# Optimization experiments

Hardware: AMD Instinct MI355X
Metric: run time of the kernel (lower is better)

The kernel has to match this reference:

```python
import jax, jax.numpy as jnp
import numpy as np

B, C, H, W = 2, 256, 64, 64
NUM_HEADS = 4
DIM_HEAD_QK = 64
DIM_HEAD_V = 64  # dim_out // num_heads
DIM_OUT_QK = NUM_HEADS * DIM_HEAD_QK  # 256
DIM_OUT_V = NUM_HEADS * DIM_HEAD_V    # 256
SCALE = DIM_HEAD_QK ** -0.5


def rel_logits_1d(q, rel_k, permute):
    # q: (Bh, Hq, Wq, d), rel_k: (2*Wq-1, d)
    Bh, Hq, Wq, d = q.shape
    R = 2 * Wq - 1
    x = jnp.einsum('bhwd,rd->bhwr', q, rel_k)              # (Bh, Hq, Wq, R)
    x = x.reshape(-1, Wq, R)
    x_pad = jnp.pad(x, ((0, 0), (0, 0), (0, 1))).reshape(x.shape[0], -1)
    x_pad = jnp.pad(x_pad, ((0, 0), (0, Wq - 1)))
    x_pad = x_pad.reshape(-1, Wq + 1, R)
    x = x_pad[:, :Wq, Wq - 1:]                              # (Bh*Hq, Wq, Wq)
    x = x.reshape(Bh, Hq, 1, Wq, Wq)
    x = jnp.broadcast_to(x, (Bh, Hq, Hq, Wq, Wq))
    return jnp.transpose(x, permute)


def pos_embed_rel(q, height_rel, width_rel):
    # q: (Bh, HW, d)
    Bh = q.shape[0]
    qr = q.reshape(Bh, H, W, -1)
    rel_w = rel_logits_1d(qr, width_rel, (0, 1, 3, 2, 4))   # (Bh, H, W, H, W)
    qt = jnp.transpose(qr, (0, 2, 1, 3))                    # (Bh, W, H, d)
    rel_h = rel_logits_1d(qt, height_rel, (0, 3, 1, 4, 2))  # (Bh, H, W, H, W)
    return (rel_h + rel_w).reshape(Bh, H * W, H * W)


def setup_inputs() -> dict:
    key = jax.random.key(0)
    k1, k2, k3, k4 = jax.random.split(key, 4)
    x = jax.random.normal(k1, (B, C, H, W), dtype=jnp.float32)
    qkv_w = jax.random.normal(k2, (2 * DIM_OUT_QK + DIM_OUT_V, C), dtype=jnp.float32) * (C ** -0.5)
    height_rel = jax.random.normal(k3, (2 * H - 1, DIM_HEAD_QK), dtype=jnp.float32) * SCALE
    width_rel = jax.random.normal(k4, (2 * W - 1, DIM_HEAD_QK), dtype=jnp.float32) * SCALE
    return {"x": x, "qkv_w": qkv_w, "height_rel": height_rel, "width_rel": width_rel}


def reference(x, qkv_w, height_rel, width_rel):
    # 1x1 conv == channel matmul
    qkv = jnp.einsum('bchw,oc->bohw', x, qkv_w)             # (B, 768, H, W)
    q, k, v = jnp.split(qkv, [DIM_OUT_QK, 2 * DIM_OUT_QK], axis=1)
    HW = H * W
    q = q.reshape(B * NUM_HEADS, DIM_HEAD_QK, HW).transpose(0, 2, 1)  # (Bh, HW, d)
    k = k.reshape(B * NUM_HEADS, DIM_HEAD_QK, HW)                     # (Bh, d, HW)
    v = v.reshape(B * NUM_HEADS, DIM_HEAD_V, HW).transpose(0, 2, 1)   # (Bh, HW, dv)
    attn = jnp.einsum('bnd,bdm->bnm', q, k) * SCALE + pos_embed_rel(q, height_rel, width_rel)
    attn = jax.nn.softmax(attn, axis=-1)
    out = jnp.einsum('bnm,bmd->bnd', attn, v)               # (Bh, HW, dv)
    out = out.transpose(0, 2, 1).reshape(B, DIM_OUT_V, H, W)
    return out
```

## Files before the change

### kernel.cpp

```cpp
#include <hip/hip_runtime.h>
#include <hip/hip_bf16.h>

typedef __attribute__((ext_vector_type(8))) short bf16x8;
typedef __attribute__((ext_vector_type(4))) float f32x4;

static __device__ __forceinline__ f32x4 mfma16(bf16x8 a, bf16x8 b, f32x4 c) {
    return __builtin_amdgcn_mfma_f32_16x16x32_bf16(a, b, c, 0, 0, 0);
}
static __device__ __forceinline__ void gll16(const void* g, void* l) {
    __builtin_amdgcn_global_load_lds(
        (const __attribute__((address_space(1))) unsigned int*)g,
        (__attribute__((address_space(3))) unsigned int*)l, 16, 0, 0);
}

#define LOG2E 1.44269504f

__global__ __launch_bounds__(256, 4) void qkv_kernel(
    const float* __restrict__ x, const float* __restrict__ w,
    __hip_bfloat16* __restrict__ qb, __hip_bfloat16* __restrict__ kb,
    __hip_bfloat16* __restrict__ vt)
{
    alignas(16) __shared__ __hip_bfloat16 sA[64 * 72];
    alignas(16) __shared__ __hip_bfloat16 sB[64 * 72];
    const int nb = blockIdx.x * 64;
    const int ob = blockIdx.y * 64;
    const int b  = blockIdx.z;
    const int tid  = threadIdx.x;
    const int lane = tid & 63;
    const int wv   = tid >> 6;
    const int quad = lane >> 4;
    const int l16  = lane & 15;

    f32x4 acc[4];
    for (int i = 0; i < 4; i++) acc[i] = (f32x4)0.f;

    const int oA = tid >> 2, cA = (tid & 3) << 4;
    const float* srcw = w + (ob + oA) * 256 + cA;
    const int cB = tid >> 2, nB = (tid & 3) << 4;
    const int csw = cB ^ ((tid & 3) * 16);
    const float* srcx = x + ((size_t)b * 256 + cB) * 4096 + nb + nB;

    float4 ra[4], rb4[4];
    #pragma unroll
    for (int i = 0; i < 4; i++) ra[i]  = *(const float4*)(srcw + i * 4);
    #pragma unroll
    for (int i = 0; i < 4; i++) rb4[i] = *(const float4*)(srcx + i * 4);

    for (int t = 0; t < 4; t++) {
        __syncthreads();
        {
            union { bf16x8 v; __hip_bfloat16 h[8]; } u0, u1;
            #pragma unroll
            for (int i = 0; i < 2; i++) {
                float4 f = ra[i];
                u0.h[4*i+0] = __float2bfloat16(f.x); u0.h[4*i+1] = __float2bfloat16(f.y);
                u0.h[4*i+2] = __float2bfloat16(f.z); u0.h[4*i+3] = __float2bfloat16(f.w);
            }
            #pragma unroll
            for (int i = 0; i < 2; i++) {
                float4 f = ra[2 + i];
                u1.h[4*i+0] = __float2bfloat16(f.x); u1.h[4*i+1] = __float2bfloat16(f.y);
                u1.h[4*i+2] = __float2bfloat16(f.z); u1.h[4*i+3] = __float2bfloat16(f.w);
            }
            *(bf16x8*)&sA[oA * 72 + cA]     = u0.v;
            *(bf16x8*)&sA[oA * 72 + cA + 8] = u1.v;
        }
        {
            #pragma unroll
            for (int i = 0; i < 4; i++) {
                float4 f = rb4[i];
                sB[(nB + 4*i + 0) * 72 + csw] = __float2bfloat16(f.x);
                sB[(nB + 4*i + 1) * 72 + csw] = __float2bfloat16(f.y);
                sB[(nB + 4*i + 2) * 72 + csw] = __float2bfloat16(f.z);
                sB[(nB + 4*i + 3) * 72 + csw] = __float2bfloat16(f.w);
            }
        }
        __syncthreads();
        if (t < 3) {
            #pragma unroll
            for (int i = 0; i < 4; i++)
                ra[i]  = *(const float4*)(srcw + (t + 1) * 64 + i * 4);
            #pragma unroll
            for (int i = 0; i < 4; i++)
                rb4[i] = *(const float4*)(srcx + (size_t)(t + 1) * 64 * 4096 + i * 4);
        }
        const __hip_bfloat16* aRow = &sA[(16 * wv + l16) * 72];
        #pragma unroll
        for (int ks = 0; ks < 2; ks++) {
            bf16x8 af = *(const bf16x8*)&aRow[ks * 32 + quad * 8];
            #pragma unroll
            for (int ct = 0; ct < 4; ct++) {
                bf16x8 bfv = *(const bf16x8*)&sB[(16 * ct + l16) * 72
                                                 + ((ks * 32 + quad * 8) ^ (ct * 16))];
                acc[ct] = mfma16(af, bfv, acc[ct]);
            }
        }
    }
    if (ob < 512) {
        __syncthreads();
        #pragma unroll
        for (int ct = 0; ct < 4; ct++) {
            union { short4 s; __hip_bfloat16 hh[4]; } u;
            #pragma unroll
            for (int r = 0; r < 4; r++) u.hh[r] = __float2bfloat16(acc[ct][r]);
            *(short4*)&sA[(16 * ct + l16) * 72 + 16 * wv + 4 * quad] = u.s;
        }
        __syncthreads();
        const int n_l = tid >> 2, d16 = (tid & 3) * 16;
        const int n = nb + n_l;
        const __hip_bfloat16* srcl = &sA[n_l * 72 + d16];
        bf16x8 v0 = *(const bf16x8*)srcl;
        bf16x8 v1 = *(const bf16x8*)(srcl + 8);
        const int bhh = b * 4 + ((ob & 255) >> 6);
        if (ob < 256) {
            __hip_bfloat16* dst = qb + ((size_t)bhh * 4096 + n) * 64;
            *(bf16x8*)(dst + d16)     = v0;
            *(bf16x8*)(dst + d16 + 8) = v1;
        } else {
            const int s = (n & 7) << 3;
            __hip_bfloat16* dst = kb + ((size_t)bhh * 4096 + n) * 64;
            *(bf16x8*)(dst + (d16 ^ s))       = v0;
            *(bf16x8*)(dst + ((d16 + 8) ^ s)) = v1;
        }
    } else {
        __syncthreads();
        #pragma unroll
        for (int ct = 0; ct < 4; ct++)
            #pragma unroll
            for (int r = 0; r < 4; r++)
                sA[(16 * wv + quad * 4 + r) * 72 + 16 * ct + l16] = __float2bfloat16(acc[ct][r]);
        int o2 = (ob - 512) + 16 * wv + l16;
        int bhh = b * 4 + (o2 >> 6), d = o2 & 63;
        const __hip_bfloat16* srcl = &sA[(16 * wv + l16) * 72 + 16 * quad];
        __hip_bfloat16* vrow = vt + ((size_t)bhh * 64 + d) * 4096;
        const int kt = quad & 1;
        const int gbase = nb + (quad >> 1) * 32;
        const int dsw = (d & 7) << 3;
        #pragma unroll
        for (int m = 0; m < 4; m++) {
            short4 val = *(const short4*)(srcl + 4 * m);
            int P4 = gbase + 8 * m + 4 * kt;
            *(short4*)(vrow + (P4 ^ dsw)) = val;
        }
    }
}

__global__ __launch_bounds__(512, 4) void attn_kernel(
    const __hip_bfloat16* __restrict__ qb, const __hip_bfloat16* __restrict__ kb,
    const __hip_bfloat16* __restrict__ vt, const float* __restrict__ hrel,
    const float* __restrict__ wrel, float* __restrict__ out)
{
    extern __shared__ __align__(16) char smem[];
    alignas(16) __shared__ __hip_bfloat16 sRH[64 * 66];

    const int h    = blockIdx.x;
    const int bh   = blockIdx.y;
    const int tid  = threadIdx.x;
    const int lane = tid & 63;
    const int wv   = tid >> 6;
    const int qg   = wv >> 2;
    const int kg   = wv & 3;
    const int quad = lane >> 4;
    const int l16  = lane & 15;

    __hip_bfloat16* sQ   = (__hip_bfloat16*)smem;
    __hip_bfloat16* sW   = (__hip_bfloat16*)smem + 64 * 72;
    __hip_bfloat16* sHRs = (__hip_bfloat16*)smem + 192 * 72;
    __hip_bfloat16* sRWt = (__hip_bfloat16*)smem;

    {
        int r = tid >> 3, d8 = (tid & 7) * 8;
        *(bf16x8*)&sQ[r * 72 + d8] =
            *(const bf16x8*)&qb[(((size_t)bh * 4096 + h * 64 + r)) * 64 + d8];
    }
    {
        int r = tid >> 2, c0 = (tid & 3) << 4;
        union { bf16x8 v; __hip_bfloat16 h8[8]; } u0, u1;
        #pragma unroll
        for (int i = 0; i < 2; i++) {
            float4 f = (r < 127) ? *(const float4*)&wrel[r * 64 + c0 + 4*i] : float4{0,0,0,0};
            u0.h8[4*i+0] = __float2bfloat16(f.x); u0.h8[4*i+1] = __float2bfloat16(f.y);
            u0.h8[4*i+2] = __float2bfloat16(f.z); u0.h8[4*i+3] = __float2bfloat16(f.w);
        }
        #pragma unroll
        for (int i = 0; i < 2; i++) {
            float4 f = (r < 127) ? *(const float4*)&wrel[r * 64 + c0 + 8 + 4*i] : float4{0,0,0,0};
            u1.h8[4*i+0] = __float2bfloat16(f.x); u1.h8[4*i+1] = __float2bfloat16(f.y);
            u1.h8[4*i+2] = __float2bfloat16(f.z); u1.h8[4*i+3] = __float2bfloat16(f.w);
        }
        *(bf16x8*)&sW[r * 72 + c0]     = u0.v;
        *(bf16x8*)&sW[r * 72 + c0 + 8] = u1.v;
    }
    {
        int r = tid >> 3, c0 = (tid & 7) * 8;
        union { bf16x8 v; __hip_bfloat16 h8[8]; } u0;
        #pragma unroll
        for (int i = 0; i < 2; i++) {
            float4 f = *(const float4*)&hrel[(63 - h + r) * 64 + c0 + 4*i];
            u0.h8[4*i+0] = __float2bfloat16(f.x); u0.h8[4*i+1] = __float2bfloat16(f.y);
            u0.h8[4*i+2] = __float2bfloat16(f.z); u0.h8[4*i+3] = __float2bfloat16(f.w);
        }
        *(bf16x8*)&sHRs[r * 72 + c0] = u0.v;
    }
    __syncthreads();

    const int g    = wv & 3;
    const int half = wv >> 2;
    const __hip_bfloat16* aRow = &sQ[(16 * g + l16) * 72];
    bf16x8 qf0 = *(const bf16x8*)&aRow[quad * 8];
    bf16x8 qf1 = *(const bf16x8*)&aRow[32 + quad * 8];
    bf16x8 qm[2][2];
    #pragma unroll
    for (int qt = 0; qt < 2; qt++) {
        const __hip_bfloat16* qr = &sQ[(qg * 32 + 16 * qt + l16) * 72];
        qm[qt][0] = *(const bf16x8*)&qr[quad * 8];
        qm[qt][1] = *(const bf16x8*)&qr[32 + quad * 8];
    }
    __syncthreads();

    {
        const int rbase = half * 64;
        #pragma unroll
        for (int ct = 0; ct < 4; ct++) {
            int rr = rbase + 16 * ct + l16;
            f32x4 a = (f32x4)0.f;
            a = mfma16(qf0, *(const bf16x8*)&sW[rr * 72 + quad * 8], a);
            a = mfma16(qf1, *(const bf16x8*)&sW[rr * 72 + 32 + quad * 8], a);
            #pragma unroll
            for (int r = 0; r < 4; r++) {
                int ww = 16 * g + quad * 4 + r;
                int wp = rr + ww - 63;
                if (wp >= 0 && wp < 64) sRWt[ww * 68 + wp] = __float2bfloat16(a[r]);
            }
        }
    }
    if (half == 0) {
        #pragma unroll
        for (int ct = 0; ct < 4; ct++) {
            f32x4 a = (f32x4)0.f;
            a = mfma16(qf0, *(const bf16x8*)&sHRs[(16 * ct + l16) * 72 + quad * 8], a);
            a = mfma16(qf1, *(const bf16x8*)&sHRs[(16 * ct + l16) * 72 + 32 + quad * 8], a);
            #pragma unroll
            for (int r = 0; r < 4; r++)
                sRH[(16 * g + quad * 4 + r) * 66 + 16 * ct + l16] = __float2bfloat16(a[r]);
        }
    }
    __syncthreads();

    union S4 { short4 s; __hip_bfloat16 h[4]; };
    float rwf[2][2][4];
    #pragma unroll
    for (int qt = 0; qt < 2; qt++)
        #pragma unroll
        for (int kt = 0; kt < 2; kt++) {
            S4 t;
            t.s = *(const short4*)&sRWt[(qg * 32 + 16 * qt + l16) * 68
                                        + 32 * (kg & 1) + 16 * kt + 4 * quad];
            #pragma unroll
            for (int r = 0; r < 4; r++)
                rwf[qt][kt][r] = LOG2E * __bfloat162float(t.h[r]);
        }
    __syncthreads();

    const char* kT = (const char*)kb + (size_t)bh * 524288 + wv * 1024 + lane * 16;
    const char* vT = (const char*)vt + (size_t)bh * 524288
                     + (size_t)(wv * 4 + quad) * 8192 + l16 * 16;

    gll16(kT,           smem + wv * 1024);
    gll16(kT + 8192,    smem + 8192 + wv * 1024);
    gll16(vT,           smem + 16384 + wv * 1024);
    gll16(vT + 262144,  smem + 24576 + wv * 1024);
    __syncthreads();

    f32x4 oacc[2][4];
    #pragma unroll
    for (int qt = 0; qt < 2; qt++)
        #pragma unroll
        for (int dt = 0; dt < 4; dt++) oacc[qt][dt] = (f32x4)0.f;
    f32x4 lacc[2] = {(f32x4)0.f, (f32x4)0.f};
    const bf16x8 vones = (bf16x8)(short)0x3F80;

    const int krowOff = (kg * 32 + l16) * 128;
    const int sw  = (l16 & 7) << 4;
    const int kA  = (quad * 16) ^ sw;
    const int kB  = (64 + quad * 16) ^ sw;
    const int vOff = 16384 + l16 * 256 + ((kg * 64 + quad * 16) ^ sw);

    const __hip_bfloat16* rh0 = &sRH[(qg * 32 + l16) * 66];
    const __hip_bfloat16* rh1 = &sRH[(qg * 32 + 16 + l16) * 66];
    const float SC = 0.125f * LOG2E;

    for (int j = 0; j < 32; j++) {
        const char* buf = smem + (j & 1) * 32768;
        if (j < 31) {
            char* nbuf = smem + ((j + 1) & 1) * 32768;
            const char* gk = kT + (size_t)(j + 1) * 16384;
            gll16(gk,          nbuf + wv * 1024);
            gll16(gk + 8192,   nbuf + 8192 + wv * 1024);
            const char* gv = vT + (size_t)(j + 1) * 256;
            gll16(gv,          nbuf + 16384 + wv * 1024);
            gll16(gv + 262144, nbuf + 24576 + wv * 1024);
        }

        const char* kr = buf + krowOff;
        bf16x8 kf00 = *(const bf16x8*)(kr + kA);
        bf16x8 kf01 = *(const bf16x8*)(kr + kB);
        bf16x8 kf10 = *(const bf16x8*)(kr + 2048 + kA);
        bf16x8 kf11 = *(const bf16x8*)(kr + 2048 + kB);

        f32x4 s[2][2];
        __builtin_amdgcn_s_setprio(1);
        #pragma unroll
        for (int qt = 0; qt < 2; qt++) {
            f32x4 a0 = (f32x4)0.f, a1 = (f32x4)0.f;
            a0 = mfma16(kf00, qm[qt][0], a0);
            a0 = mfma16(kf01, qm[qt][1], a0);
            a1 = mfma16(kf10, qm[qt][0], a1);
            a1 = mfma16(kf11, qm[qt][1], a1);
            s[qt][0] = a0; s[qt][1] = a1;
        }
        __builtin_amdgcn_s_setprio(0);

        const int hp = 2 * j + (kg >> 1);
        bf16x8 pa[2];
        #pragma unroll
        for (int qt = 0; qt < 2; qt++) {
            float rhb = LOG2E * __bfloat162float((qt ? rh1 : rh0)[hp]);
            float pv[8];
            #pragma unroll
            for (int r = 0; r < 4; r++)
                pv[r] = __builtin_amdgcn_exp2f(fmaf(s[qt][0][r], SC, rwf[qt][0][r] + rhb));
            #pragma unroll
            for (int r = 0; r < 4; r++)
                pv[4 + r] = __builtin_amdgcn_exp2f(fmaf(s[qt][1][r], SC, rwf[qt][1][r] + rhb));
            union { bf16x8 v; __hip_bfloat162 b2[4]; } pu;
            #pragma unroll
            for (int pi = 0; pi < 4; pi++)
                pu.b2[pi] = __float22bfloat162_rn(float2{pv[2 * pi], pv[2 * pi + 1]});
            pa[qt] = pu.v;
        }

        __builtin_amdgcn_s_setprio(1);
        #pragma unroll
        for (int dt = 0; dt < 4; dt++) {
            bf16x8 vf = *(const bf16x8*)(buf + vOff + dt * 4096);
            oacc[0][dt] = mfma16(pa[0], vf, oacc[0][dt]);
            oacc[1][dt] = mfma16(pa[1], vf, oacc[1][dt]);
        }
        lacc[0] = mfma16(pa[0], vones, lacc[0]);
        lacc[1] = mfma16(pa[1], vones, lacc[1]);
        __builtin_amdgcn_s_setprio(0);
        __syncthreads();
    }

    float* obuf = (float*)smem;
    if (kg != 0) {
        float* rb = obuf + (kg - 1) * 4672;
        #pragma unroll
        for (int qt = 0; qt < 2; qt++)
            #pragma unroll
            for (int dt = 0; dt < 4; dt++)
                *(f32x4*)&rb[qg * 2304 + (16 * dt + l16) * 36 + 16 * qt + 4 * quad]
                    = oacc[qt][dt];
        if (l16 == 0)
            #pragma unroll
            for (int qt = 0; qt < 2; qt++)
                #pragma unroll
                for (int r = 0; r < 4; r++)
                    rb[4608 + qg * 32 + 16 * qt + 4 * quad + r] = lacc[qt][r];
    }
    __syncthreads();
    if (kg == 0) {
        #pragma unroll
        for (int rg = 0; rg < 3; rg++) {
            const float* rb = obuf + rg * 4672;
            #pragma unroll
            for (int qt = 0; qt < 2; qt++) {
                #pragma unroll
                for (int dt = 0; dt < 4; dt++)
                    oacc[qt][dt] += *(const f32x4*)&rb[qg * 2304 + (16 * dt + l16) * 36
                                                       + 16 * qt + 4 * quad];
                #pragma unroll
                for (int r = 0; r < 4; r++)
                    lacc[qt][r] += rb[4608 + qg * 32 + 16 * qt + 4 * quad + r];
            }
        }
        const int b = bh >> 2, head = bh & 3;
        #pragma unroll
        for (int qt = 0; qt < 2; qt++) {
            f32x4 lv;
            #pragma unroll
            for (int r = 0; r < 4; r++) lv[r] = 1.f / lacc[qt][r];
            #pragma unroll
            for (int dt = 0; dt < 4; dt++) {
                f32x4 o = oacc[qt][dt] * lv;
                int dv = 16 * dt + l16;
                int q0 = qg * 32 + 16 * qt + 4 * quad;
                *(f32x4*)&out[((size_t)(b * 256 + head * 64 + dv)) * 4096 + h * 64 + q0] = o;
            }
        }
    }
}

extern "C" void kernel_launch(void* const* d_in, const int* in_sizes, int n_in,
                              void* d_out, int out_size, void* d_ws, size_t ws_size,
                              hipStream_t stream) {
    const float* x     = (const float*)d_in[0];
    const float* qkv_w = (const float*)d_in[1];
    const float* hrel  = (const float*)d_in[2];
    const float* wrel  = (const float*)d_in[3];
    float* out = (float*)d_out;

    __hip_bfloat16* qb = (__hip_bfloat16*)d_ws;
    __hip_bfloat16* kb = qb + (size_t)8 * 4096 * 64;
    __hip_bfloat16* vt = kb + (size_t)8 * 4096 * 64;

    qkv_kernel<<<dim3(64, 12, 2), 256, 0, stream>>>(x, qkv_w, qb, kb, vt);
    attn_kernel<<<dim3(64, 8), 512, 65536, stream>>>(qb, kb, vt, hrel, wrel, out);
}
```

Before: 126.8 us.

## Halve attention block to 256 threads with two key groups and smaller LDS

The attention kernel moves from 8 waves (2 query groups x 4 key groups) to 4 waves (2 x 2), and halves the double-buffered K/V tile to 64 keys per iteration over 64 iterations. Dynamic LDS drops from 64KB to 32KB and the final cross-wave reduction covers only one partner group. The aim is to fit more blocks per CU and cut reduction overhead. The cost is half as many waves per block to hide latency, twice as many loop iterations and barriers, and relative-position tables built in two passes.

Measured after the change: 130.2 us. +2.7%, slower.

```diff
diff --git a/kernel.cpp b/kernel.cpp
--- a/kernel.cpp
+++ b/kernel.cpp
@@ -11,6 +11,14 @@
     __builtin_amdgcn_global_load_lds(
         (const __attribute__((address_space(1))) unsigned int*)g,
         (__attribute__((address_space(3))) unsigned int*)l, 16, 0, 0);
+}
+static __device__ __forceinline__ bf16x8 pack8(float4 a, float4 b) {
+    union { bf16x8 v; __hip_bfloat162 h[4]; } u;
+    u.h[0] = __float22bfloat162_rn(float2{a.x, a.y});
+    u.h[1] = __float22bfloat162_rn(float2{a.z, a.w});
+    u.h[2] = __float22bfloat162_rn(float2{b.x, b.y});
+    u.h[3] = __float22bfloat162_rn(float2{b.z, b.w});
+    return u.v;
 }
 
 #define LOG2E 1.44269504f
@@ -145,68 +153,43 @@
     }
 }
 
-__global__ __launch_bounds__(512, 4) void attn_kernel(
+__global__ __launch_bounds__(256, 4) void attn_kernel(
     const __hip_bfloat16* __restrict__ qb, const __hip_bfloat16* __restrict__ kb,
     const __hip_bfloat16* __restrict__ vt, const float* __restrict__ hrel,
     const float* __restrict__ wrel, float* __restrict__ out)
 {
     extern __shared__ __align__(16) char smem[];
-    alignas(16) __shared__ __hip_bfloat16 sRH[64 * 66];
+    __shared__ __hip_bfloat16 sRH[64 * 64];
 
     const int h    = blockIdx.x;
     const int bh   = blockIdx.y;
     const int tid  = threadIdx.x;
     const int lane = tid & 63;
     const int wv   = tid >> 6;
-    const int qg   = wv >> 2;
-    const int kg   = wv & 3;
+    const int qg   = wv >> 1;
+    const int kg   = wv & 1;
     const int quad = lane >> 4;
     const int l16  = lane & 15;
 
     __hip_bfloat16* sQ   = (__hip_bfloat16*)smem;
     __hip_bfloat16* sW   = (__hip_bfloat16*)smem + 64 * 72;
-    __hip_bfloat16* sHRs = (__hip_bfloat16*)smem + 192 * 72;
+    __hip_bfloat16* sHRs = (__hip_bfloat16*)smem + 128 * 72;
     __hip_bfloat16* sRWt = (__hip_bfloat16*)smem;
 
     {
-        int r = tid >> 3, d8 = (tid & 7) * 8;
-        *(bf16x8*)&sQ[r * 72 + d8] =
-            *(const bf16x8*)&qb[(((size_t)bh * 4096 + h * 64 + r)) * 64 + d8];
-    }
-    {
-        int r = tid >> 2, c0 = (tid & 3) << 4;
-        union { bf16x8 v; __hip_bfloat16 h8[8]; } u0, u1;
-        #pragma unroll
-        for (int i = 0; i < 2; i++) {
-            float4 f = (r < 127) ? *(const float4*)&wrel[r * 64 + c0 + 4*i] : float4{0,0,0,0};
-            u0.h8[4*i+0] = __float2bfloat16(f.x); u0.h8[4*i+1] = __float2bfloat16(f.y);
-            u0.h8[4*i+2] = __float2bfloat16(f.z); u0.h8[4*i+3] = __float2bfloat16(f.w);
-        }
-        #pragma unroll
-        for (int i = 0; i < 2; i++) {
-            float4 f = (r < 127) ? *(const float4*)&wrel[r * 64 + c0 + 8 + 4*i] : float4{0,0,0,0};
-            u1.h8[4*i+0] = __float2bfloat16(f.x); u1.h8[4*i+1] = __float2bfloat16(f.y);
-            u1.h8[4*i+2] = __float2bfloat16(f.z); u1.h8[4*i+3] = __float2bfloat16(f.w);
-        }
-        *(bf16x8*)&sW[r * 72 + c0]     = u0.v;
-        *(bf16x8*)&sW[r * 72 + c0 + 8] = u1.v;
-    }
-    {
-        int r = tid >> 3, c0 = (tid & 7) * 8;
-        union { bf16x8 v; __hip_bfloat16 h8[8]; } u0;
-        #pragma unroll
-        for (int i = 0; i < 2; i++) {
-            float4 f = *(const float4*)&hrel[(63 - h + r) * 64 + c0 + 4*i];
-            u0.h8[4*i+0] = __float2bfloat16(f.x); u0.h8[4*i+1] = __float2bfloat16(f.y);
-            u0.h8[4*i+2] = __float2bfloat16(f.z); u0.h8[4*i+3] = __float2bfloat16(f.w);
-        }
-        *(bf16x8*)&sHRs[r * 72 + c0] = u0.v;
+        int r = tid >> 2, c0 = (tid & 3) * 16;
+        const __hip_bfloat16* srcq = qb + ((size_t)bh * 4096 + h * 64 + r) * 64 + c0;
+        *(bf16x8*)&sQ[r * 72 + c0]     = *(const bf16x8*)srcq;
+        *(bf16x8*)&sQ[r * 72 + c0 + 8] = *(const bf16x8*)(srcq + 8);
+        const float* srch = hrel + (size_t)(63 - h + r) * 64 + c0;
+        *(bf16x8*)&sHRs[r * 72 + c0]     = pack8(*(const float4*)srch,
+                                                 *(const float4*)(srch + 4));
+        *(bf16x8*)&sHRs[r * 72 + c0 + 8] = pack8(*(const float4*)(srch + 8),
+                                                 *(const float4*)(srch + 12));
     }
     __syncthreads();
 
-    const int g    = wv & 3;
-    const int half = wv >> 2;
-    const __hip_bfloat16* aRow = &sQ[(16 * g + l16) * 72];
+    const __hip_bfloat16* aRow = &sQ[(16 * wv + l16) * 72];
     bf16x8 qf0 = *(const bf16x8*)&aRow[quad * 8];
     bf16x8 qf1 = *(const bf16x8*)&aRow[32 + quad * 8];
     bf16x8 qm[2][2];
@@ -218,34 +201,46 @@
     }
     __syncthreads();
 
-    {
-        const int rbase = half * 64;
+    for (int p = 0; p < 2; p++) {
+        {
+            int r = tid >> 2, c0 = (tid & 3) * 16;
+            int gr = 64 * p + r;
+            bf16x8 w0 = (bf16x8)(short)0, w1 = (bf16x8)(short)0;
+            if (gr < 127) {
+                const float* s = wrel + (size_t)gr * 64 + c0;
+                w0 = pack8(*(const float4*)s, *(const float4*)(s + 4));
+                w1 = pack8(*(const float4*)(s + 8), *(const float4*)(s + 12));
+            }
+            *(bf16x8*)&sW[r * 72 + c0]     = w0;
+            *(bf16x8*)&sW[r * 72 + c0 + 8] = w1;
+        }
+        __syncthreads();
         #pragma unroll
         for (int ct = 0; ct < 4; ct++) {
-            int rr = rbase + 16 * ct + l16;
             f32x4 a = (f32x4)0.f;
-            a = mfma16(qf0, *(const bf16x8*)&sW[rr * 72 + quad * 8], a);
-            a = mfma16(qf1, *(const bf16x8*)&sW[rr * 72 + 32 + quad * 8], a);
+            a = mfma16(qf0, *(const bf16x8*)&sW[(16 * ct + l16) * 72 + quad * 8], a);
+            a = mfma16(qf1, *(const bf16x8*)&sW[(16 * ct + l16) * 72 + 32 + quad * 8], a);
+            int rr = 64 * p + 16 * ct + l16;
             #pragma unroll
             for (int r = 0; r < 4; r++) {
-                int ww = 16 * g + quad * 4 + r;
+                int ww = 16 * wv + quad * 4 + r;
                 int wp = rr + ww - 63;
                 if (wp >= 0 && wp < 64) sRWt[ww * 68 + wp] = __float2bfloat16(a[r]);
             }
         }
-    }
-    if (half == 0) {
-        #pragma unroll
-        for (int ct = 0; ct < 4; ct++) {
-            f32x4 a = (f32x4)0.f;
-            a = mfma16(qf0, *(const bf16x8*)&sHRs[(16 * ct + l16) * 72 + quad * 8], a);
-            a = mfma16(qf1, *(const bf16x8*)&sHRs[(16 * ct + l16) * 72 + 32 + quad * 8], a);
-            #pragma unroll
-            for (int r = 0; r < 4; r++)
-                sRH[(16 * g + quad * 4 + r) * 66 + 16 * ct + l16] = __float2bfloat16(a[r]);
-        }
-    }
-    __syncthreads();
+        if (p == 0) {
+            #pragma unroll
+            for (int ct = 0; ct < 4; ct++) {
+                f32x4 a = (f32x4)0.f;
+                a = mfma16(qf0, *(const bf16x8*)&sHRs[(16 * ct + l16) * 72 + quad * 8], a);
+                a = mfma16(qf1, *(const bf16x8*)&sHRs[(16 * ct + l16) * 72 + 32 + quad * 8], a);
+                #pragma unroll
+                for (int r = 0; r < 4; r++)
+                    sRH[(16 * ct + l16) * 64 + 16 * wv + quad * 4 + r] = __float2bfloat16(a[r]);
+            }
+        }
+        __syncthreads();
+    }
 
     union S4 { short4 s; __hip_bfloat16 h[4]; };
     float rwf[2][2][4];
@@ -255,21 +250,21 @@
         for (int kt = 0; kt < 2; kt++) {
             S4 t;
             t.s = *(const short4*)&sRWt[(qg * 32 + 16 * qt + l16) * 68
-                                        + 32 * (kg & 1) + 16 * kt + 4 * quad];
+                                        + kg * 32 + 16 * kt + 4 * quad];
             #pragma unroll
             for (int r = 0; r < 4; r++)
                 rwf[qt][kt][r] = LOG2E * __bfloat162float(t.h[r]);
         }
     __syncthreads();
 
-    const char* kT = (const char*)kb + (size_t)bh * 524288 + wv * 1024 + lane * 16;
+    const char* kT = (const char*)kb + (size_t)bh * 524288 + wv * 2048 + lane * 16;
     const char* vT = (const char*)vt + (size_t)bh * 524288
-                     + (size_t)(wv * 4 + quad) * 8192 + l16 * 16;
-
-    gll16(kT,           smem + wv * 1024);
-    gll16(kT + 8192,    smem + 8192 + wv * 1024);
-    gll16(vT,           smem + 16384 + wv * 1024);
-    gll16(vT + 262144,  smem + 24576 + wv * 1024);
+                     + (size_t)(16 * wv + (lane >> 3)) * 8192 + (lane & 7) * 16;
+
+    gll16(kT,          smem + wv * 2048);
+    gll16(kT + 1024,   smem + wv * 2048 + 1024);
+    gll16(vT,          smem + 8192 + wv * 2048);
+    gll16(vT + 65536,  smem + 8192 + wv * 2048 + 1024);
     __syncthreads();
 
     f32x4 oacc[2][4];
@@ -284,22 +279,21 @@
     const int sw  = (l16 & 7) << 4;
     const int kA  = (quad * 16) ^ sw;
     const int kB  = (64 + quad * 16) ^ sw;
-    const int vOff = 16384 + l16 * 256 + ((kg * 64 + quad * 16) ^ sw);
-
-    const __hip_bfloat16* rh0 = &sRH[(qg * 32 + l16) * 66];
-    const __hip_bfloat16* rh1 = &sRH[(qg * 32 + 16 + l16) * 66];
+    const int vOff = 8192 + l16 * 128 + ((kg * 64 + quad * 16) ^ sw);
+
+    const __hip_bfloat16* rhq = sRH + qg * 32 + l16;
     const float SC = 0.125f * LOG2E;
 
-    for (int j = 0; j < 32; j++) {
-        const char* buf = smem + (j & 1) * 32768;
-        if (j < 31) {
-            char* nbuf = smem + ((j + 1) & 1) * 32768;
-            const char* gk = kT + (size_t)(j + 1) * 16384;
-            gll16(gk,          nbuf + wv * 1024);
-            gll16(gk + 8192,   nbuf + 8192 + wv * 1024);
-            const char* gv = vT + (size_t)(j + 1) * 256;
-            gll16(gv,          nbuf + 16384 + wv * 1024);
-            gll16(gv + 262144, nbuf + 24576 + wv * 1024);
+    for (int j = 0; j < 64; j++) {
+        const char* buf = smem + (j & 1) * 16384;
+        if (j < 63) {
+            char* nbuf = smem + ((j + 1) & 1) * 16384;
+            const char* gk = kT + (size_t)(j + 1) * 8192;
+            gll16(gk,         nbuf + wv * 2048);
+            gll16(gk + 1024,  nbuf + wv * 2048 + 1024);
+            const char* gv = vT + (size_t)(j + 1) * 128;
+            gll16(gv,         nbuf + 8192 + wv * 2048);
+            gll16(gv + 65536, nbuf + 8192 + wv * 2048 + 1024);
         }
 
         const char* kr = buf + krowOff;
@@ -321,11 +315,10 @@
         }
         __builtin_amdgcn_s_setprio(0);
 
-        const int hp = 2 * j + (kg >> 1);
         bf16x8 pa[2];
         #pragma unroll
         for (int qt = 0; qt < 2; qt++) {
-            float rhb = LOG2E * __bfloat162float((qt ? rh1 : rh0)[hp]);
+            float rhb = LOG2E * __bfloat162float(rhq[j * 64 + 16 * qt]);
             float pv[8];
             #pragma unroll
             for (int r = 0; r < 4; r++)
@@ -343,7 +336,7 @@
         __builtin_amdgcn_s_setprio(1);
         #pragma unroll
         for (int dt = 0; dt < 4; dt++) {
-            bf16x8 vf = *(const bf16x8*)(buf + vOff + dt * 4096);
+            bf16x8 vf = *(const bf16x8*)(buf + vOff + dt * 2048);
             oacc[0][dt] = mfma16(pa[0], vf, oacc[0][dt]);
             oacc[1][dt] = mfma16(pa[1], vf, oacc[1][dt]);
         }
@@ -354,36 +347,31 @@
     }
 
     float* obuf = (float*)smem;
-    if (kg != 0) {
-        float* rb = obuf + (kg - 1) * 4672;
+    if (kg == 1) {
         #pragma unroll
         for (int qt = 0; qt < 2; qt++)
             #pragma unroll
             for (int dt = 0; dt < 4; dt++)
-                *(f32x4*)&rb[qg * 2304 + (16 * dt + l16) * 36 + 16 * qt + 4 * quad]
+                *(f32x4*)&obuf[qg * 2304 + (16 * dt + l16) * 36 + 16 * qt + 4 * quad]
                     = oacc[qt][dt];
         if (l16 == 0)
             #pragma unroll
             for (int qt = 0; qt < 2; qt++)
                 #pragma unroll
                 for (int r = 0; r < 4; r++)
-                    rb[4608 + qg * 32 + 16 * qt + 4 * quad + r] = lacc[qt][r];
+                    obuf[4608 + qg * 32 + 16 * qt + 4 * quad + r] = lacc[qt][r];
     }
     __syncthreads();
     if (kg == 0) {
         #pragma unroll
-        for (int rg = 0; rg < 3; rg++) {
-            const float* rb = obuf + rg * 4672;
-            #pragma unroll
-            for (int qt = 0; qt < 2; qt++) {
-                #pragma unroll
-                for (int dt = 0; dt < 4; dt++)
-                    oacc[qt][dt] += *(const f32x4*)&rb[qg * 2304 + (16 * dt + l16) * 36
-                                                       + 16 * qt + 4 * quad];
-                #pragma unroll
-                for (int r = 0; r < 4; r++)
-                    lacc[qt][r] += rb[4608 + qg * 32 + 16 * qt + 4 * quad + r];
-            }
+        for (int qt = 0; qt < 2; qt++) {
+            #pragma unroll
+            for (int dt = 0; dt < 4; dt++)
+                oacc[qt][dt] += *(const f32x4*)&obuf[qg * 2304 + (16 * dt + l16) * 36
+                                                     + 16 * qt + 4 * quad];
+            #pragma unroll
+            for (int r = 0; r < 4; r++)
+                lacc[qt][r] += obuf[4608 + qg * 32 + 16 * qt + 4 * quad + r];
         }
         const int b = bh >> 2, head = bh & 3;
         #pragma unroll
@@ -416,5 +404,5 @@
     __hip_bfloat16* vt = kb + (size_t)8 * 4096 * 64;
 
     qkv_kernel<<<dim3(64, 12, 2), 256, 0, stream>>>(x, qkv_w, qb, kb, vt);
-    attn_kernel<<<dim3(64, 8), 512, 65536, stream>>>(qb, kb, vt, hrel, wrel, out);
-}
+    attn_kernel<<<dim3(64, 8), 256, 32768, stream>>>(qb, kb, vt, hrel, wrel, out);
+}
```
